# Kernel optimization log

Hardware: AMD Instinct MI355X
Metric: run time of the kernel (lower is better)

The kernel has to match this reference:

```python
import jax, jax.numpy as jnp
import numpy as np

N = 4096
IN_F = 512
OUT_F = 64
HEADS = 4
ALPHA = 0.2  # leaky relu slope
NEG_INF = -9e15


def setup_inputs() -> dict:
    key = jax.random.key(0)
    k1, k2, k3, k4 = jax.random.split(key, 4)
    x = jax.random.normal(k1, (N, IN_F), dtype=jnp.float32)
    adj = jax.random.randint(k2, (N, N), 0, 2, dtype=jnp.int32)
    # xavier-uniform-like init for params
    limW = float(np.sqrt(6.0 / (IN_F + OUT_F * HEADS)))
    W = jax.random.uniform(k3, (IN_F, OUT_F * HEADS), dtype=jnp.float32, minval=-limW, maxval=limW)
    lima = float(np.sqrt(6.0 / (2 * OUT_F + 1)))
    a = jax.random.uniform(k4, (2 * OUT_F, 1), dtype=jnp.float32, minval=-lima, maxval=lima)
    return {"x": x, "adj": adj, "W": W, "a": a}


def reference(x, adj, W, a):
    # h: [N, H, F]
    h = (x @ W).reshape(N, HEADS, OUT_F)
    a_src = a[:OUT_F, 0]   # [F]
    a_dst = a[OUT_F:, 0]   # [F]
    s = jnp.einsum("nhf,f->nh", h, a_src)  # source-node score [N, H]
    t = jnp.einsum("nhf,f->nh", h, a_dst)  # dest-node score   [N, H]
    # e[i, j, k] = leaky_relu(s[i,k] + t[j,k]) -> [N, N, H]
    e = jax.nn.leaky_relu(s[:, None, :] + t[None, :, :], negative_slope=ALPHA)
    mask = (adj > 0)[:, :, None]  # [N, N, 1]
    e = jnp.where(mask, e, NEG_INF)
    attn = jax.nn.softmax(e, axis=1)  # softmax over neighbors j
    # weighted aggregation per head: [N, H, F]
    h_prime = jnp.einsum("ijh,jhf->ihf", attn, h)
    return h_prime.reshape(N, HEADS * OUT_F)
```

## Files before the change

### kernel.cpp

```cpp
#include <hip/hip_runtime.h>
#include <hip/hip_bf16.h>


#define NN 4096
#define KF 512
#define NF 256

typedef __attribute__((ext_vector_type(8))) short bf16x8;
typedef __attribute__((ext_vector_type(4))) short s16x4;
typedef __attribute__((ext_vector_type(4))) float f32x4;

union AB8 { bf16x8 v; short2 h[4]; short s[8]; int4 i4; };
union ST4 { s16x4 v; short2 h[2]; };
union I64 { long v; int i[2]; };

__device__ __forceinline__ short f2bf(float f) {
    union { float f; unsigned u; } v; v.f = f;
    unsigned r = v.u + 0x7fffu + ((v.u >> 16) & 1u);
    return (short)(r >> 16);
}
__device__ __forceinline__ float bf2f(short b) {
    union { unsigned u; float f; } v;
    v.u = ((unsigned)(unsigned short)b) << 16;
    return v.f;
}
__device__ __forceinline__ short2 pkbf(float a, float b) {
    __hip_bfloat162 t = __float22bfloat162_rn(make_float2(a, b));
    union { __hip_bfloat162 v; short2 s; } u; u.v = t;
    return u.s;
}
__device__ __forceinline__ int pkfp8x4(float a, float b, float c, float d) {
    int p = __builtin_amdgcn_cvt_pk_fp8_f32(a, b, 0, false);
    p     = __builtin_amdgcn_cvt_pk_fp8_f32(c, d, p, true);
    return p;
}

__global__ __launch_bounds__(256) void wpack(const float* __restrict__ W,
                                             short* __restrict__ WtF) {
    int tid = blockIdx.x * 256 + threadIdx.x;
    int l = tid & 63, nt = (tid >> 6) & 3, hd = (tid >> 8) & 3, kblk = tid >> 10;
    int q = l >> 4, r = l & 15;
    int col = hd * 64 + nt * 16 + r;
    int k0 = kblk * 32 + q * 8;
    AB8 o;
    #pragma unroll
    for (int e = 0; e < 8; e++) o.s[e] = f2bf(W[(k0 + e) * NF + col]);
    *(bf16x8*)(WtF + (size_t)tid * 8) = o.v;
}

__global__ __launch_bounds__(256) void adjpack(const int* __restrict__ adj,
                                               unsigned* __restrict__ pT) {
    int gw   = (blockIdx.x * 256 + threadIdx.x) >> 6;
    int lane = threadIdx.x & 63;
    int i = gw >> 4, seg = gw & 15;
    const int* ap = adj + (size_t)i * NN + seg * 256 + lane;
    unsigned long long b0 = __ballot(ap[0]   != 0);
    unsigned long long b1 = __ballot(ap[64]  != 0);
    unsigned long long b2 = __ballot(ap[128] != 0);
    unsigned long long b3 = __ballot(ap[192] != 0);
    if (lane == 0) {
        *(uint4*)(pT + ((size_t)(seg * 2    ) * NN + i) * 4) =
            make_uint4((unsigned)b0, (unsigned)(b0 >> 32), (unsigned)b1, (unsigned)(b1 >> 32));
        *(uint4*)(pT + ((size_t)(seg * 2 + 1) * NN + i) * 4) =
            make_uint4((unsigned)b2, (unsigned)(b2 >> 32), (unsigned)b3, (unsigned)(b3 >> 32));
    }
}

__global__ __launch_bounds__(256) void gemm(const float* __restrict__ x,
                                            const short* __restrict__ WtF,
                                            short* __restrict__ VtF,
                                            unsigned char* __restrict__ VtF8) {
    const int lane = threadIdx.x & 63, wv = threadIdx.x >> 6;
    const int q = lane >> 4, r = lane & 15;
    const int i0 = blockIdx.x * 64 + wv * 16;
    const int hd = blockIdx.y >> 1, ntp = (blockIdx.y & 1) * 2;

    const float* xp = x + (size_t)(i0 + r) * KF + q * 8;
    const short* wp = WtF + ((size_t)((hd * 4 + ntp) * 64 + lane)) * 8;

    f32x4 acc0 = {}, acc1 = {};
    #pragma unroll 4
    for (int kb = 0; kb < 16; kb++) {
        float4 xa = *(const float4*)(xp + kb * 32);
        float4 xb2 = *(const float4*)(xp + kb * 32 + 4);
        AB8 av;
        av.h[0] = pkbf(xa.x, xa.y);  av.h[1] = pkbf(xa.z, xa.w);
        av.h[2] = pkbf(xb2.x, xb2.y); av.h[3] = pkbf(xb2.z, xb2.w);
        bf16x8 b0 = *(const bf16x8*)(wp + kb * 8192);
        bf16x8 b1 = *(const bf16x8*)(wp + kb * 8192 + 512);
        acc0 = __builtin_amdgcn_mfma_f32_16x16x32_bf16(av.v, b0, acc0, 0, 0, 0);
        acc1 = __builtin_amdgcn_mfma_f32_16x16x32_bf16(av.v, b1, acc1, 0, 0, 0);
    }
    const int jblk = i0 >> 5;
    const int base = (i0 & 16) + q * 4;
    const int qa = base >> 3, e0 = base & 7;
    ST4 s0, s1;
    s0.h[0] = pkbf(acc0[0], acc0[1]); s0.h[1] = pkbf(acc0[2], acc0[3]);
    s1.h[0] = pkbf(acc1[0], acc1[1]); s1.h[1] = pkbf(acc1[2], acc1[3]);
    const size_t slot0 = (size_t)(((jblk * 4 + hd) * 4 + ntp    ) * 64 + qa * 16 + r);
    const size_t slot1 = (size_t)(((jblk * 4 + hd) * 4 + ntp + 1) * 64 + qa * 16 + r);
    *(s16x4*)(VtF + slot0 * 8 + e0) = s0.v;
    *(s16x4*)(VtF + slot1 * 8 + e0) = s1.v;
    *(int*)(VtF8 + slot0 * 8 + e0) = pkfp8x4(acc0[0], acc0[1], acc0[2], acc0[3]);
    *(int*)(VtF8 + slot1 * 8 + e0) = pkfp8x4(acc1[0], acc1[1], acc1[2], acc1[3]);
}

__global__ __launch_bounds__(256) void prep(const short* __restrict__ VtF,
                                            const float* __restrict__ a,
                                            float* __restrict__ ipk,
                                            float2* __restrict__ jpk) {
    const int l = threadIdx.x & 63, hd = threadIdx.x >> 6;
    const int q = l >> 4, r = l & 15;
    const int jblk = blockIdx.x;
    float as[4], at[4];
    #pragma unroll
    for (int nt = 0; nt < 4; nt++) { as[nt] = a[nt * 16 + r]; at[nt] = a[64 + nt * 16 + r]; }
    float ps[8] = {}, pt[8] = {};
    #pragma unroll
    for (int nt = 0; nt < 4; nt++) {
        AB8 hv; hv.v = *(const bf16x8*)(VtF + ((size_t)(((jblk * 4 + hd) * 4 + nt) * 64 + l)) * 8);
        #pragma unroll
        for (int e = 0; e < 8; e++) { float v = bf2f(hv.s[e]); ps[e] += v * as[nt]; pt[e] += v * at[nt]; }
    }
    #pragma unroll
    for (int d = 1; d < 16; d <<= 1) {
        #pragma unroll
        for (int e = 0; e < 8; e++) { ps[e] += __shfl_xor(ps[e], d, 64); pt[e] += __shfl_xor(pt[e], d, 64); }
    }
    if (r == 0) {
        #pragma unroll
        for (int e = 0; e < 8; e++) {
            int j = jblk * 32 + q * 8 + e;
            ipk[hd * NN + j] = __expf(-0.8f * ps[e]);
            jpk[hd * NN + j] = make_float2(__expf(pt[e]), __expf(0.2f * pt[e]));
        }
    }
}

struct PF { float4 ja, jb, jc, jd; long v0, v1, v2, v3; };

__global__ __launch_bounds__(1024) __attribute__((amdgpu_waves_per_eu(1, 4)))
void gat_attn(const uint4* __restrict__ pT4, const float* __restrict__ ipk,
              const float* __restrict__ jpkf, const unsigned char* __restrict__ VtF8,
              float* __restrict__ out) {
    const int tid = threadIdx.x, lane = tid & 63, wv = tid >> 6;
    const int hd = wv & 3, jq = wv >> 2;
    const int q = lane >> 4, r = lane & 15;
    const int i0 = blockIdx.x * 16, i = i0 + r;
    const float ci = ipk[hd * NN + i];
    const int qs = q * 8;
    const float* jpf = jpkf + (size_t)hd * NN * 2;

    f32x4 acc[5] = {};
    const long ones = 0x3838383838383838L;

    auto load_pf = [&](PF& p, int it) {
        const float4* jp = (const float4*)(jpf + 2 * ((jq << 10) + (it << 5) + qs));
        p.ja = jp[0]; p.jb = jp[1]; p.jc = jp[2]; p.jd = jp[3];
        const long* vp = (const long*)(VtF8 + (size_t)(((jq * 32 + it) * 16 + hd * 4) * 512) + lane * 8);
        p.v0 = vp[0]; p.v1 = vp[64]; p.v2 = vp[128]; p.v3 = vp[192];
    };
    auto consume = [&](const PF& p, unsigned w) {
        float p0 = (w & 1u)   ? fmaxf(p.ja.x, ci * p.ja.y) : 0.f;
        float p1 = (w & 2u)   ? fmaxf(p.ja.z, ci * p.ja.w) : 0.f;
        float p2 = (w & 4u)   ? fmaxf(p.jb.x, ci * p.jb.y) : 0.f;
        float p3 = (w & 8u)   ? fmaxf(p.jb.z, ci * p.jb.w) : 0.f;
        float p4 = (w & 16u)  ? fmaxf(p.jc.x, ci * p.jc.y) : 0.f;
        float p5 = (w & 32u)  ? fmaxf(p.jc.z, ci * p.jc.w) : 0.f;
        float p6 = (w & 64u)  ? fmaxf(p.jd.x, ci * p.jd.y) : 0.f;
        float p7 = (w & 128u) ? fmaxf(p.jd.z, ci * p.jd.w) : 0.f;
        I64 af;
        af.i[0] = pkfp8x4(p0, p1, p2, p3);
        af.i[1] = pkfp8x4(p4, p5, p6, p7);
        acc[0] = __builtin_amdgcn_mfma_f32_16x16x32_fp8_fp8(af.v, p.v0, acc[0], 0, 0, 0);
        acc[1] = __builtin_amdgcn_mfma_f32_16x16x32_fp8_fp8(af.v, p.v1, acc[1], 0, 0, 0);
        acc[2] = __builtin_amdgcn_mfma_f32_16x16x32_fp8_fp8(af.v, p.v2, acc[2], 0, 0, 0);
        acc[3] = __builtin_amdgcn_mfma_f32_16x16x32_fp8_fp8(af.v, p.v3, acc[3], 0, 0, 0);
        acc[4] = __builtin_amdgcn_mfma_f32_16x16x32_fp8_fp8(af.v, ones, acc[4], 0, 0, 0);
    };

    const uint4* prow = pT4 + (size_t)(jq * 8) * NN + i;
    uint4 wg = prow[0];
    PF pa, pb;
    load_pf(pa, 0);
    #pragma unroll 1
    for (int g = 0; g < 8; g++) {
        uint4 wgn = wg;
        if (g < 7) wgn = prow[(size_t)(g + 1) * NN];
        const int it = g * 4;
        load_pf(pb, it + 1); consume(pa, wg.x >> qs);
        load_pf(pa, it + 2); consume(pb, wg.y >> qs);
        load_pf(pb, it + 3); consume(pa, wg.z >> qs);
        if (g < 7) load_pf(pa, it + 4);
        consume(pb, wg.w >> qs);
        wg = wgn;
    }

    __shared__ float sacc[3][4][5][64][4];
    if (jq > 0) {
        const int gg = jq - 1;
        #pragma unroll
        for (int t = 0; t < 5; t++)
            *(f32x4*)&sacc[gg][hd][t][lane][0] = acc[t];
    }
    __syncthreads();
    if (jq == 0) {
        #pragma unroll
        for (int gg = 0; gg < 3; gg++)
            #pragma unroll
            for (int t = 0; t < 5; t++) {
                f32x4 o = *(const f32x4*)&sacc[gg][hd][t][lane][0];
                acc[t][0] += o[0]; acc[t][1] += o[1];
                acc[t][2] += o[2]; acc[t][3] += o[3];
            }
        #pragma unroll
        for (int reg = 0; reg < 4; reg++) {
            float inv = 1.f / acc[4][reg];
            int row = i0 + q * 4 + reg;
            #pragma unroll
            for (int t = 0; t < 4; t++)
                out[(size_t)row * NF + hd * 64 + t * 16 + r] = acc[t][reg] * inv;
        }
    }
}

extern "C" void kernel_launch(void* const* d_in, const int* in_sizes, int n_in,
                              void* d_out, int out_size, void* d_ws, size_t ws_size,
                              hipStream_t stream) {
    const float* x   = (const float*)d_in[0];
    const int*   adj = (const int*)d_in[1];
    const float* W   = (const float*)d_in[2];
    const float* a   = (const float*)d_in[3];
    float* out = (float*)d_out;

    char* ws = (char*)d_ws;
    short*         WtF  = (short*)ws;
    short*         VtF  = (short*)(ws + 262144);
    unsigned char* VtF8 = (unsigned char*)(ws + 2359296);
    unsigned*      pT   = (unsigned*)(ws + 3407872);
    float*         ipk  = (float*)(ws + 5505024);
    float2*        jpk  = (float2*)(ws + 5570560);

    wpack  <<<64, 256, 0, stream>>>(W, WtF);
    adjpack<<<16384, 256, 0, stream>>>(adj, pT);
    gemm   <<<dim3(64, 8), 256, 0, stream>>>(x, WtF, VtF, VtF8);
    prep   <<<128, 256, 0, stream>>>(VtF, a, ipk, jpk);
    gat_attn<<<256, 1024, 0, stream>>>((const uint4*)pT, ipk, (const float*)jpk, VtF8, out);
}
```

Baseline: 152.7 us.

## Fuse score projection into GEMM epilogue and pre-pack x to bf16 MFMA layout

Adds an xpack kernel that converts x to bf16 in MFMA fragment layout. The GEMM is restructured so each wave computes a full head (4 n-tiles), which lets the attention-score dot products with a_src and a_dst be done in the epilogue from fp32 accumulators. This removes the separate prep kernel and the bf16 VtF intermediate write and read. The cost is an extra launch plus a 4 MB bf16 x buffer round trip, and the scores now come from fp32 rather than bf16-rounded values.

```diff
diff --git a/kernel.cpp b/kernel.cpp
--- a/kernel.cpp
+++ b/kernel.cpp
@@ -19,11 +19,6 @@
     unsigned r = v.u + 0x7fffu + ((v.u >> 16) & 1u);
     return (short)(r >> 16);
 }
-__device__ __forceinline__ float bf2f(short b) {
-    union { unsigned u; float f; } v;
-    v.u = ((unsigned)(unsigned short)b) << 16;
-    return v.f;
-}
 __device__ __forceinline__ short2 pkbf(float a, float b) {
     __hip_bfloat162 t = __float22bfloat162_rn(make_float2(a, b));
     union { __hip_bfloat162 v; short2 s; } u; u.v = t;
@@ -33,6 +28,22 @@
     int p = __builtin_amdgcn_cvt_pk_fp8_f32(a, b, 0, false);
     p     = __builtin_amdgcn_cvt_pk_fp8_f32(c, d, p, true);
     return p;
+}
+
+__global__ __launch_bounds__(256) void xpack(const float* __restrict__ x,
+                                             short* __restrict__ xF) {
+    const int lane = threadIdx.x & 63, wv = threadIdx.x >> 6;
+    const int i = blockIdx.x * 4 + wv;
+    const float4* xp = (const float4*)(x + (size_t)i * KF + lane * 8);
+    float4 xa = xp[0], xb = xp[1];
+    ST4 o0, o1;
+    o0.h[0] = pkbf(xa.x, xa.y); o0.h[1] = pkbf(xa.z, xa.w);
+    o1.h[0] = pkbf(xb.x, xb.y); o1.h[1] = pkbf(xb.z, xb.w);
+    const int kblk = lane >> 2, qk = lane & 3;
+    const int jgrp = i >> 4, r = i & 15;
+    short* dst = xF + ((size_t)(kblk * 256 + jgrp) * 64 + qk * 16 + r) * 8;
+    *(s16x4*)dst = o0.v;
+    *(s16x4*)(dst + 4) = o1.v;
 }
 
 __global__ __launch_bounds__(256) void wpack(const float* __restrict__ W,
@@ -66,73 +77,65 @@
     }
 }
 
-__global__ __launch_bounds__(256) void gemm(const float* __restrict__ x,
-                                            const short* __restrict__ WtF,
-                                            short* __restrict__ VtF,
-                                            unsigned char* __restrict__ VtF8) {
+__global__ __launch_bounds__(256) void gemmfuse(const short* __restrict__ xF,
+                                                const short* __restrict__ WtF,
+                                                const float* __restrict__ a,
+                                                unsigned char* __restrict__ VtF8,
+                                                float* __restrict__ ipk,
+                                                float2* __restrict__ jpk) {
     const int lane = threadIdx.x & 63, wv = threadIdx.x >> 6;
     const int q = lane >> 4, r = lane & 15;
-    const int i0 = blockIdx.x * 64 + wv * 16;
-    const int hd = blockIdx.y >> 1, ntp = (blockIdx.y & 1) * 2;
-
-    const float* xp = x + (size_t)(i0 + r) * KF + q * 8;
-    const short* wp = WtF + ((size_t)((hd * 4 + ntp) * 64 + lane)) * 8;
-
-    f32x4 acc0 = {}, acc1 = {};
-    #pragma unroll 4
-    for (int kb = 0; kb < 16; kb++) {
-        float4 xa = *(const float4*)(xp + kb * 32);
-        float4 xb2 = *(const float4*)(xp + kb * 32 + 4);
-        AB8 av;
-        av.h[0] = pkbf(xa.x, xa.y);  av.h[1] = pkbf(xa.z, xa.w);
-        av.h[2] = pkbf(xb2.x, xb2.y); av.h[3] = pkbf(xb2.z, xb2.w);
-        bf16x8 b0 = *(const bf16x8*)(wp + kb * 8192);
-        bf16x8 b1 = *(const bf16x8*)(wp + kb * 8192 + 512);
-        acc0 = __builtin_amdgcn_mfma_f32_16x16x32_bf16(av.v, b0, acc0, 0, 0, 0);
-        acc1 = __builtin_amdgcn_mfma_f32_16x16x32_bf16(av.v, b1, acc1, 0, 0, 0);
-    }
-    const int jblk = i0 >> 5;
-    const int base = (i0 & 16) + q * 4;
+    const int jb32 = blockIdx.x >> 1, ch = blockIdx.x & 1;
+    const int rg = wv >> 1, hd = ch * 2 + (wv & 1);
+    const int jgrp = jb32 * 2 + rg;
+
+    const short* ap = xF  + ((size_t)jgrp * 64 + lane) * 8;
+    const short* wp = WtF + ((size_t)(hd * 4) * 64 + lane) * 8;
+
+    f32x4 acc[4] = {};
+    #pragma unroll
+    for (int kblk = 0; kblk < 16; kblk++) {
+        bf16x8 av = *(const bf16x8*)(ap + (size_t)kblk * 256 * 512);
+        const short* w = wp + (size_t)kblk * 16 * 512;
+        #pragma unroll
+        for (int nt = 0; nt < 4; nt++) {
+            bf16x8 bv = *(const bf16x8*)(w + nt * 512);
+            acc[nt] = __builtin_amdgcn_mfma_f32_16x16x32_bf16(av, bv, acc[nt], 0, 0, 0);
+        }
+    }
+
+    const int base = rg * 16 + q * 4;
     const int qa = base >> 3, e0 = base & 7;
-    ST4 s0, s1;
-    s0.h[0] = pkbf(acc0[0], acc0[1]); s0.h[1] = pkbf(acc0[2], acc0[3]);
-    s1.h[0] = pkbf(acc1[0], acc1[1]); s1.h[1] = pkbf(acc1[2], acc1[3]);
-    const size_t slot0 = (size_t)(((jblk * 4 + hd) * 4 + ntp    ) * 64 + qa * 16 + r);
-    const size_t slot1 = (size_t)(((jblk * 4 + hd) * 4 + ntp + 1) * 64 + qa * 16 + r);
-    *(s16x4*)(VtF + slot0 * 8 + e0) = s0.v;
-    *(s16x4*)(VtF + slot1 * 8 + e0) = s1.v;
-    *(int*)(VtF8 + slot0 * 8 + e0) = pkfp8x4(acc0[0], acc0[1], acc0[2], acc0[3]);
-    *(int*)(VtF8 + slot1 * 8 + e0) = pkfp8x4(acc1[0], acc1[1], acc1[2], acc1[3]);
-}
-
-__global__ __launch_bounds__(256) void prep(const short* __restrict__ VtF,
-                                            const float* __restrict__ a,
-                                            float* __restrict__ ipk,
-                                            float2* __restrict__ jpk) {
-    const int l = threadIdx.x & 63, hd = threadIdx.x >> 6;
-    const int q = l >> 4, r = l & 15;
-    const int jblk = blockIdx.x;
+    #pragma unroll
+    for (int nt = 0; nt < 4; nt++) {
+        size_t slot = (size_t)(((jb32 * 4 + hd) * 4 + nt) * 64 + qa * 16 + r);
+        *(int*)(VtF8 + slot * 8 + e0) = pkfp8x4(acc[nt][0], acc[nt][1], acc[nt][2], acc[nt][3]);
+    }
+
     float as[4], at[4];
     #pragma unroll
     for (int nt = 0; nt < 4; nt++) { as[nt] = a[nt * 16 + r]; at[nt] = a[64 + nt * 16 + r]; }
-    float ps[8] = {}, pt[8] = {};
-    #pragma unroll
-    for (int nt = 0; nt < 4; nt++) {
-        AB8 hv; hv.v = *(const bf16x8*)(VtF + ((size_t)(((jblk * 4 + hd) * 4 + nt) * 64 + l)) * 8);
-        #pragma unroll
-        for (int e = 0; e < 8; e++) { float v = bf2f(hv.s[e]); ps[e] += v * as[nt]; pt[e] += v * at[nt]; }
-    }
-    #pragma unroll
-    for (int d = 1; d < 16; d <<= 1) {
-        #pragma unroll
-        for (int e = 0; e < 8; e++) { ps[e] += __shfl_xor(ps[e], d, 64); pt[e] += __shfl_xor(pt[e], d, 64); }
-    }
+    f32x4 sp = {}, tp = {};
+    #pragma unroll
+    for (int nt = 0; nt < 4; nt++)
+        #pragma unroll
+        for (int reg = 0; reg < 4; reg++) {
+            sp[reg] += acc[nt][reg] * as[nt];
+            tp[reg] += acc[nt][reg] * at[nt];
+        }
+    #pragma unroll
+    for (int d = 1; d < 16; d <<= 1)
+        #pragma unroll
+        for (int reg = 0; reg < 4; reg++) {
+            sp[reg] += __shfl_xor(sp[reg], d, 64);
+            tp[reg] += __shfl_xor(tp[reg], d, 64);
+        }
     if (r == 0) {
         #pragma unroll
-        for (int e = 0; e < 8; e++) {
-            int j = jblk * 32 + q * 8 + e;
-            ipk[hd * NN + j] = __expf(-0.8f * ps[e]);
-            jpk[hd * NN + j] = make_float2(__expf(pt[e]), __expf(0.2f * pt[e]));
+        for (int reg = 0; reg < 4; reg++) {
+            int j = jb32 * 32 + rg * 16 + q * 4 + reg;
+            ipk[hd * NN + j] = __expf(-0.8f * sp[reg]);
+            jpk[hd * NN + j] = make_float2(__expf(tp[reg]), __expf(0.2f * tp[reg]));
         }
     }
 }
@@ -234,16 +237,16 @@
     float* out = (float*)d_out;
 
     char* ws = (char*)d_ws;
-    short*         WtF  = (short*)ws;
-    short*         VtF  = (short*)(ws + 262144);
-    unsigned char* VtF8 = (unsigned char*)(ws + 2359296);
-    unsigned*      pT   = (unsigned*)(ws + 3407872);
-    float*         ipk  = (float*)(ws + 5505024);
-    float2*        jpk  = (float2*)(ws + 5570560);
-
-    wpack  <<<64, 256, 0, stream>>>(W, WtF);
-    adjpack<<<16384, 256, 0, stream>>>(adj, pT);
-    gemm   <<<dim3(64, 8), 256, 0, stream>>>(x, WtF, VtF, VtF8);
-    prep   <<<128, 256, 0, stream>>>(VtF, a, ipk, jpk);
+    short*         xF   = (short*)ws;
+    short*         WtF  = (short*)(ws + 4194304);
+    unsigned char* VtF8 = (unsigned char*)(ws + 4456448);
+    unsigned*      pT   = (unsigned*)(ws + 5505024);
+    float*         ipk  = (float*)(ws + 7602176);
+    float2*        jpk  = (float2*)(ws + 7667712);
+
+    xpack   <<<1024, 256, 0, stream>>>(x, xF);
+    wpack   <<<64, 256, 0, stream>>>(W, WtF);
+    adjpack <<<16384, 256, 0, stream>>>(adj, pT);
+    gemmfuse<<<256, 256, 0, stream>>>(xF, WtF, a, VtF8, ipk, jpk);
     gat_attn<<<256, 1024, 0, stream>>>((const uint4*)pT, ipk, (const float*)jpk, VtF8, out);
 }
```

Result: no change. 150.1 us (-1.7%).
